# Kernel optimization log

Measured on AMD Instinct MI355X. Metric: run time of the kernel, lower is better.

Reference implementation:

```python
import jax, jax.numpy as jnp
import numpy as np

N = 100000; E = 1600000; G = 512; L = 1000
FXD = 4; FXT = 5; H = 64; NOUT = 2

def setup_inputs() -> dict:
    key = jax.random.key(0)
    ks = jax.random.split(key, 16)
    x = jax.random.normal(ks[0], (N, FXD), dtype=jnp.float32)
    edge_index = jax.random.randint(ks[1], (2, E), 0, N, dtype=jnp.int64)
    # contiguous, non-empty graph assignment (sorted)
    batch = jnp.minimum(jnp.arange(N, dtype=jnp.int64) // (N // G), G - 1)
    target = jax.random.normal(ks[2], (G, L, FXT), dtype=jnp.float32)
    def lin(k, fi, fo):
        s = 1.0 / np.sqrt(fi)
        k1, k2 = jax.random.split(k)
        return (jax.random.uniform(k1, (fi, fo), jnp.float32, -s, s),
                jax.random.uniform(k2, (fo,), jnp.float32, -s, s))
    W1, b1 = lin(ks[3], FXD, H)
    W2, b2 = lin(ks[4], H, 2 * H)
    Wg, bg = lin(ks[5], 2 * H, H)
    s = 1.0 / np.sqrt(FXT * 3)
    Wc = jax.random.uniform(ks[6], (H, FXT, 3), jnp.float32, -s, s)  # OIH
    bc = jax.random.uniform(ks[7], (H,), jnp.float32, -s, s)
    Wt, bt = lin(ks[8], H, H)
    Wf, bf = lin(ks[9], 2 * H, H)
    Wo, bo = lin(ks[10], H, NOUT)
    return dict(x=x, edge_index=edge_index, batch=batch, target=target,
                W1=W1, b1=b1, W2=W2, b2=b2, Wg=Wg, bg=bg,
                Wc=Wc, bc=bc, Wt=Wt, bt=bt, Wf=Wf, bf=bf, Wo=Wo, bo=bo)

def _gcn_prep(edge_index):
    # add self-loops, compute symmetric normalization (PyG gcn_norm)
    loops = jnp.arange(N, dtype=edge_index.dtype)
    row = jnp.concatenate([edge_index[0], loops])
    col = jnp.concatenate([edge_index[1], loops])
    deg = jax.ops.segment_sum(jnp.ones_like(col, dtype=jnp.float32), col, num_segments=N)
    dis = jnp.where(deg > 0, jax.lax.rsqrt(deg), 0.0)
    norm = dis[row] * dis[col]  # [E+N]
    return row, col, norm

def _gcn_conv(h, row, col, norm):
    # gather-scale-scatter aggregation
    msg = h[row] * norm[:, None]
    return jax.ops.segment_sum(msg, col, num_segments=N)

def reference(x, edge_index, batch, target, W1, b1, W2, b2, Wg, bg, Wc, bc, Wt, bt, Wf, bf, Wo, bo):
    row, col, norm = _gcn_prep(edge_index)
    h = jax.nn.relu(_gcn_conv(x @ W1, row, col, norm) + b1)
    h = jax.nn.relu(_gcn_conv(h @ W2, row, col, norm) + b2)
    g = jax.ops.segment_max(h, batch, num_segments=G)  # global_max_pool [G, 2H]
    g = g @ Wg + bg  # dropout = identity (eval)
    t = jnp.transpose(target, (0, 2, 1))  # [G, FXT, L]
    t = jax.lax.conv_general_dilated(t, Wc, (1,), 'VALID',
                                     dimension_numbers=('NCH', 'OIH', 'NCH')) + bc[None, :, None]
    t = jax.nn.relu(t)
    t = jnp.max(t, axis=-1)  # AdaptiveMaxPool1d(1) [G, H]
    t = t @ Wt + bt
    xc = jnp.concatenate([g, t], axis=1)
    xc = jax.nn.relu(xc @ Wf + bf)
    return xc @ Wo + bo
```

## Files before the change

### kernel.cpp

```cpp
#include <hip/hip_runtime.h>
#include <hip/hip_bf16.h>

constexpr int N   = 100000;
constexpr int E   = 1600000;
constexpr int G   = 512;
constexpr int L   = 1000;
constexpr int NPG = 195;

constexpr int SLOTS = 48;
constexpr int NR2   = 256;
constexpr int RS2   = 391;
constexpr int PCAP2 = 6912;
constexpr int BCH   = 4096;
constexpr int NBP   = (E + BCH - 1) / BCH;

typedef __attribute__((ext_vector_type(8))) short bf16x8;
typedef __attribute__((ext_vector_type(4))) float f32x4;

__device__ __forceinline__ float bf2f(__hip_bfloat16 b) { return __bfloat162float(b); }
__device__ __forceinline__ float lo_bf(unsigned v) { return __uint_as_float(v << 16); }
__device__ __forceinline__ float hi_bf(unsigned v) { return __uint_as_float(v & 0xFFFF0000u); }
__device__ __forceinline__ unsigned packbf2(float a, float b) {
    __hip_bfloat16 ha = __float2bfloat16(a), hb = __float2bfloat16(b);
    unsigned short ua = *(unsigned short*)&ha, ub = *(unsigned short*)&hb;
    return (unsigned)ua | ((unsigned)ub << 16);
}

struct SMPart { unsigned rec[BCH]; unsigned char rr[BCH];
                int cnt[NR2]; int base[NR2]; int cur[NR2]; };
struct SMConv { float tg[L * 5]; float pm[4 * 64]; };


__global__ void __launch_bounds__(256) k_part_conv(
        const int* __restrict__ row, const int* __restrict__ col,
        int* __restrict__ pcnt, unsigned* __restrict__ precs,
        const float* __restrict__ target, const float* __restrict__ Wc,
        const float* __restrict__ bc, float* __restrict__ tb,
        const float* __restrict__ W2, short* __restrict__ W2hi,
        short* __restrict__ W2lo) {
    __shared__ __align__(16) char smbuf[sizeof(SMPart) > sizeof(SMConv)
                                        ? sizeof(SMPart) : sizeof(SMConv)];
    int tid = threadIdx.x;
    int bid = blockIdx.x;
    if (bid < NBP) {
        SMPart& sp = *reinterpret_cast<SMPart*>(smbuf);
        sp.cnt[tid] = 0;
        __syncthreads();
        int e0 = bid * BCH;
        int nE = min(BCH, E - e0);
        for (int i = tid; i < nE; i += 256) {
            int c = __builtin_nontemporal_load(col + e0 + i);
            int r = __builtin_nontemporal_load(row + e0 + i);
            int rr = c / RS2;
            sp.rec[i] = ((unsigned)r << 9) | (unsigned)(c - rr * RS2);
            sp.rr[i] = (unsigned char)rr;
            atomicAdd(&sp.cnt[rr], 1);
        }
        __syncthreads();
        sp.base[tid] = atomicAdd(&pcnt[tid], sp.cnt[tid]);
        sp.cur[tid] = 0;
        __syncthreads();
        for (int i = tid; i < nE; i += 256) {
            int rr = sp.rr[i];
            int p = sp.base[rr] + atomicAdd(&sp.cur[rr], 1);
            if (p < PCAP2) precs[rr * PCAP2 + p] = sp.rec[i];
        }
    } else if (bid < NBP + G) {
        SMConv& sc = *reinterpret_cast<SMConv*>(smbuf);
        int gi = bid - NBP;
        const float* tsrc = target + (size_t)gi * (L * 5);
        for (int i = tid; i < L * 5; i += 256) sc.tg[i] = tsrc[i];
        __syncthreads();
        int co = tid & 63, rr = tid >> 6;
        float wc[15];
        #pragma unroll
        for (int j = 0; j < 15; j++) wc[j] = Wc[co * 15 + j];
        const float* tg = sc.tg;
        int p0 = rr * 250;
        int pend = min(p0 + 250, 998);
        float a0 = tg[p0 * 5 + 0], a1 = tg[p0 * 5 + 1], a2 = tg[p0 * 5 + 2],
              a3 = tg[p0 * 5 + 3], a4 = tg[p0 * 5 + 4];
        float b0 = tg[p0 * 5 + 5], b1 = tg[p0 * 5 + 6], b2 = tg[p0 * 5 + 7],
              b3 = tg[p0 * 5 + 8], b4 = tg[p0 * 5 + 9];
        float m = -1e30f;
        for (int p = p0; p < pend; p++) {
            const float* cp = &tg[(p + 2) * 5];
            float c0 = cp[0], c1 = cp[1], c2 = cp[2], c3 = cp[3], c4 = cp[4];
            float v = 0.0f;
            v = fmaf(a0, wc[0],  v); v = fmaf(b0, wc[1],  v); v = fmaf(c0, wc[2],  v);
            v = fmaf(a1, wc[3],  v); v = fmaf(b1, wc[4],  v); v = fmaf(c1, wc[5],  v);
            v = fmaf(a2, wc[6],  v); v = fmaf(b2, wc[7],  v); v = fmaf(c2, wc[8],  v);
            v = fmaf(a3, wc[9],  v); v = fmaf(b3, wc[10], v); v = fmaf(c3, wc[11], v);
            v = fmaf(a4, wc[12], v); v = fmaf(b4, wc[13], v); v = fmaf(c4, wc[14], v);
            m = fmaxf(m, v);
            a0 = b0; a1 = b1; a2 = b2; a3 = b3; a4 = b4;
            b0 = c0; b1 = c1; b2 = c2; b3 = c3; b4 = c4;
        }
        sc.pm[rr * 64 + co] = m;
        __syncthreads();
        if (tid < 64) {
            float mm = fmaxf(fmaxf(sc.pm[tid], sc.pm[64 + tid]),
                             fmaxf(sc.pm[128 + tid], sc.pm[192 + tid]));
            tb[gi * 64 + tid] = fmaxf(mm + bc[tid], 0.0f);
        }
    } else {
        int i = (bid - NBP - G) * 256 + tid;
        if (i < 64 * 128) {
            float w = W2[i];
            __hip_bfloat16 h = __float2bfloat16(w);
            float r = w - __bfloat162float(h);
            __hip_bfloat16 l = __float2bfloat16(r);
            W2hi[i] = *(short*)&h;
            W2lo[i] = *(short*)&l;
        }
    }
}


__global__ void __launch_bounds__(256) k_sort(
        const int* __restrict__ pcnt, const unsigned* __restrict__ precs,
        int* __restrict__ slots, int* __restrict__ cursor, float* __restrict__ dis) {
    __shared__ int cnt2[RS2];
    int tid = threadIdx.x;
    int rr = blockIdx.x;
    int cnt = min(pcnt[rr], PCAP2);
    for (int i = tid; i < RS2; i += 256) cnt2[i] = 0;
    __syncthreads();
    const unsigned* pr = precs + rr * PCAP2;
    for (int i = tid; i < cnt; i += 256) {
        unsigned r = pr[i];
        int ln = (int)(r & 511u);
        int j = atomicAdd(&cnt2[ln], 1);
        if (j < SLOTS) slots[(rr * RS2 + ln) * SLOTS + j] = (int)(r >> 9);
    }
    __syncthreads();
    for (int ln = tid; ln < RS2; ln += 256) {
        int n = rr * RS2 + ln;
        if (n < N) {
            int c = cnt2[ln];
            dis[n] = rsqrtf((float)c + 1.0f);
            cursor[n] = n * SLOTS + min(c, SLOTS);
        }
    }
}


__global__ void __launch_bounds__(256) k_gxl1(
        const int* __restrict__ cursor, const int* __restrict__ slots,
        const float* __restrict__ dis, const float4* __restrict__ x,
        const float* __restrict__ W1, const float* __restrict__ b1,
        unsigned* __restrict__ h32) {
    __shared__ float ax[64][4];
    __shared__ float w1s[256];
    __shared__ float b1s[64];
    int tid = threadIdx.x;
    w1s[tid] = W1[tid];
    if (tid < 64) b1s[tid] = b1[tid];
    int nb = blockIdx.x * 64;
    int ln = tid >> 2, sub = tid & 3;
    int n = nb + ln;
    float4 a = make_float4(0.f, 0.f, 0.f, 0.f);
    if (n < N) {
        int s = n * SLOTS;
        int cnt = cursor[n] - s;
        for (int j = sub; j < cnt; j += 4) {
            int sx = slots[s + j];
            float w = dis[sx];
            float4 v = x[sx];
            a.x = fmaf(v.x, w, a.x); a.y = fmaf(v.y, w, a.y);
            a.z = fmaf(v.z, w, a.z); a.w = fmaf(v.w, w, a.w);
        }
    }
    a.x += __shfl_xor(a.x, 1); a.y += __shfl_xor(a.y, 1);
    a.z += __shfl_xor(a.z, 1); a.w += __shfl_xor(a.w, 1);
    a.x += __shfl_xor(a.x, 2); a.y += __shfl_xor(a.y, 2);
    a.z += __shfl_xor(a.z, 2); a.w += __shfl_xor(a.w, 2);
    if (sub == 0 && n < N) {
        float dn = dis[n];
        float sl = dn * dn;
        float4 xs = x[n];
        ax[ln][0] = fmaf(xs.x, sl, a.x * dn);
        ax[ln][1] = fmaf(xs.y, sl, a.y * dn);
        ax[ln][2] = fmaf(xs.z, sl, a.z * dn);
        ax[ln][3] = fmaf(xs.w, sl, a.w * dn);
    }
    __syncthreads();
    int p = tid & 31, r0 = tid >> 5;
    int f0 = 2 * p, f1 = 2 * p + 1;
    float wA0 = w1s[f0],       wB0 = w1s[f1];
    float wA1 = w1s[64 + f0],  wB1 = w1s[64 + f1];
    float wA2 = w1s[128 + f0], wB2 = w1s[128 + f1];
    float wA3 = w1s[192 + f0], wB3 = w1s[192 + f1];
    float bb0 = b1s[f0], bb1 = b1s[f1];
    #pragma unroll
    for (int i = 0; i < 8; i++) {
        int l2 = r0 + 8 * i;
        int node = nb + l2;
        if (node >= N) break;
        float v0 = bb0, v1 = bb1;
        float g0 = ax[l2][0], g1 = ax[l2][1], g2 = ax[l2][2], g3 = ax[l2][3];
        v0 = fmaf(g0, wA0, v0); v1 = fmaf(g0, wB0, v1);
        v0 = fmaf(g1, wA1, v0); v1 = fmaf(g1, wB1, v1);
        v0 = fmaf(g2, wA2, v0); v1 = fmaf(g2, wB2, v1);
        v0 = fmaf(g3, wA3, v0); v1 = fmaf(g3, wB3, v1);
        h32[(size_t)node * 32 + p] = packbf2(fmaxf(v0, 0.0f), fmaxf(v1, 0.0f));
    }
}


__global__ void __launch_bounds__(256) k_gather_h(
        const int* __restrict__ cursor, const int* __restrict__ slots,
        const float* __restrict__ dis, const unsigned* __restrict__ h32,
        unsigned* __restrict__ aggh32) {
    __shared__ int2 lsw[8][SLOTS];
    __shared__ int  lcnt[8];
    int tid = threadIdx.x;
    int nb = blockIdx.x * 8;
    if (tid < 8) {
        int node = nb + tid;
        lcnt[tid] = (node < N) ? (cursor[node] - node * SLOTS) : 0;
    }
    __syncthreads();
    for (int i = tid; i < 8 * SLOTS; i += 256) {
        int lo = i / SLOTS, j = i - lo * SLOTS;
        if (j < lcnt[lo]) {
            int src = slots[(nb + lo) * SLOTS + j];
            lsw[lo][j] = make_int2(src, __float_as_int(dis[src]));
        }
    }
    __syncthreads();
    int wid = tid >> 6, lane = tid & 63;
    int half = lane >> 5, li = lane & 31;
    int local = wid * 2 + half;
    int n = nb + local;
    if (n >= N) return;
    int cnt = lcnt[local];
    float dn = dis[n];
    float acc0 = 0.0f, acc1 = 0.0f;
    int j = 0;
    for (; j + 16 <= cnt; j += 16) {
        unsigned v[16]; float w[16];
        #pragma unroll
        for (int k = 0; k < 16; k++) {
            int2 e = lsw[local][j + k];
            v[k] = h32[(size_t)e.x * 32 + li];
            w[k] = __int_as_float(e.y);
        }
        #pragma unroll
        for (int k = 0; k < 16; k++) {
            acc0 = fmaf(w[k], lo_bf(v[k]), acc0);
            acc1 = fmaf(w[k], hi_bf(v[k]), acc1);
        }
    }
    for (; j + 4 <= cnt; j += 4) {
        unsigned v[4]; float w[4];
        #pragma unroll
        for (int k = 0; k < 4; k++) {
            int2 e = lsw[local][j + k];
            v[k] = h32[(size_t)e.x * 32 + li];
            w[k] = __int_as_float(e.y);
        }
        #pragma unroll
        for (int k = 0; k < 4; k++) {
            acc0 = fmaf(w[k], lo_bf(v[k]), acc0);
            acc1 = fmaf(w[k], hi_bf(v[k]), acc1);
        }
    }
    for (; j < cnt; j++) {
        int2 e = lsw[local][j];
        unsigned v = h32[(size_t)e.x * 32 + li];
        float w = __int_as_float(e.y);
        acc0 = fmaf(w, lo_bf(v), acc0);
        acc1 = fmaf(w, hi_bf(v), acc1);
    }
    unsigned sv = h32[(size_t)n * 32 + li];
    acc0 = fmaf(dn, lo_bf(sv), acc0) * dn;
    acc1 = fmaf(dn, hi_bf(sv), acc1) * dn;
    aggh32[(size_t)n * 32 + li] = packbf2(acc0, acc1);
}


__global__ void __launch_bounds__(256) k_mfma_pool(
        const __hip_bfloat16* __restrict__ aggh,
        const short* __restrict__ W2hi, const short* __restrict__ W2lo,
        const float* __restrict__ b2, const float* __restrict__ tb,
        const float* __restrict__ Wg, const float* __restrict__ bg,
        const float* __restrict__ Wt, const float* __restrict__ bt,
        const float* __restrict__ Wf, const float* __restrict__ bf,
        const float* __restrict__ Wo, const float* __restrict__ bo,
        float* __restrict__ out) {
    __shared__ float gvec[128], ts[64], g2s[64], t2s[64], xcs[64];
    int tid = threadIdx.x;
    int wid = tid >> 6, lane = tid & 63;
    int m = lane & 15, quad = lane >> 4;
    int gi = blockIdx.x;
    int n0 = gi * NPG;
    int n1 = (gi == G - 1) ? N : n0 + NPG;
    int cb0 = wid * 32, cb1 = cb0 + 16;
    bf16x8 bh[2][2], bl[2][2];
    #pragma unroll
    for (int t = 0; t < 2; t++) {
        int cb = cb0 + t * 16;
        #pragma unroll
        for (int ks = 0; ks < 2; ks++) {
            bf16x8 hh, ll;
            #pragma unroll
            for (int j = 0; j < 8; j++) {
                int k = ks * 32 + quad * 8 + j;
                hh[j] = W2hi[k * 128 + cb + m];
                ll[j] = W2lo[k * 128 + cb + m];
            }
            bh[t][ks] = hh; bl[t][ks] = ll;
        }
    }
    float bias0 = b2[cb0 + m], bias1 = b2[cb1 + m];
    const short* ah = (const short*)aggh;
    float mx0 = 0.0f, mx1 = 0.0f;
    bf16x8 a0, a1;
    {
        const short* p = ah + (size_t)(n0 + m) * 64 + quad * 8;
        a0 = *(const bf16x8*)p;
        a1 = *(const bf16x8*)(p + 32);
    }
    for (int bn = n0; bn < n1; bn += 16) {
        bf16x8 na0 = a0, na1 = a1;
        if (bn + 16 < n1) {
            const short* p = ah + (size_t)(bn + 16 + m) * 64 + quad * 8;
            na0 = *(const bf16x8*)p;
            na1 = *(const bf16x8*)(p + 32);
        }
        f32x4 acc0 = {0.f, 0.f, 0.f, 0.f};
        f32x4 acc1 = {0.f, 0.f, 0.f, 0.f};
        acc0 = __builtin_amdgcn_mfma_f32_16x16x32_bf16(a0, bh[0][0], acc0, 0, 0, 0);
        acc0 = __builtin_amdgcn_mfma_f32_16x16x32_bf16(a1, bh[0][1], acc0, 0, 0, 0);
        acc0 = __builtin_amdgcn_mfma_f32_16x16x32_bf16(a0, bl[0][0], acc0, 0, 0, 0);
        acc0 = __builtin_amdgcn_mfma_f32_16x16x32_bf16(a1, bl[0][1], acc0, 0, 0, 0);
        acc1 = __builtin_amdgcn_mfma_f32_16x16x32_bf16(a0, bh[1][0], acc1, 0, 0, 0);
        acc1 = __builtin_amdgcn_mfma_f32_16x16x32_bf16(a1, bh[1][1], acc1, 0, 0, 0);
        acc1 = __builtin_amdgcn_mfma_f32_16x16x32_bf16(a0, bl[1][0], acc1, 0, 0, 0);
        acc1 = __builtin_amdgcn_mfma_f32_16x16x32_bf16(a1, bl[1][1], acc1, 0, 0, 0);
        int rb = bn + quad * 4;
        #pragma unroll
        for (int r = 0; r < 4; r++) {
            float v0 = fmaxf(acc0[r] + bias0, 0.0f);
            float v1 = fmaxf(acc1[r] + bias1, 0.0f);
            if (rb + r < n1) {
                mx0 = fmaxf(mx0, v0);
                mx1 = fmaxf(mx1, v1);
            }
        }
        a0 = na0; a1 = na1;
    }
    mx0 = fmaxf(mx0, __shfl_xor(mx0, 16));
    mx0 = fmaxf(mx0, __shfl_xor(mx0, 32));
    mx1 = fmaxf(mx1, __shfl_xor(mx1, 16));
    mx1 = fmaxf(mx1, __shfl_xor(mx1, 32));
    if (quad == 0) {
        gvec[cb0 + m] = mx0;
        gvec[cb1 + m] = mx1;
    }
    __syncthreads();
    if (wid == 0) {
        ts[lane] = tb[gi * 64 + lane];
        float a = bg[lane];
        #pragma unroll 8
        for (int k = 0; k < 128; k++) a = fmaf(gvec[k], Wg[k * 64 + lane], a);
        float b = bt[lane];
        #pragma unroll 8
        for (int k = 0; k < 64; k++) b = fmaf(ts[k], Wt[k * 64 + lane], b);
        g2s[lane] = a;
        t2s[lane] = b;
        float c = bf[lane];
        #pragma unroll 8
        for (int k = 0; k < 64; k++) c = fmaf(g2s[k], Wf[k * 64 + lane], c);
        #pragma unroll 8
        for (int k = 0; k < 64; k++) c = fmaf(t2s[k], Wf[(64 + k) * 64 + lane], c);
        xcs[lane] = fmaxf(c, 0.0f);
        if (lane < 2) {
            float o = bo[lane];
            for (int k = 0; k < 64; k++) o = fmaf(xcs[k], Wo[k * 2 + lane], o);
            out[gi * 2 + lane] = o;
        }
    }
}


extern "C" void kernel_launch(void* const* d_in, const int* in_sizes, int n_in,
                              void* d_out, int out_size, void* d_ws, size_t ws_size,
                              hipStream_t stream) {
    const float* x      = (const float*)d_in[0];
    const int*   ei     = (const int*)d_in[1];
    const float* target = (const float*)d_in[3];
    const float* W1 = (const float*)d_in[4];
    const float* b1 = (const float*)d_in[5];
    const float* W2 = (const float*)d_in[6];
    const float* b2 = (const float*)d_in[7];
    const float* Wg = (const float*)d_in[8];
    const float* bg = (const float*)d_in[9];
    const float* Wc = (const float*)d_in[10];
    const float* bc = (const float*)d_in[11];
    const float* Wt = (const float*)d_in[12];
    const float* bt = (const float*)d_in[13];
    const float* Wf = (const float*)d_in[14];
    const float* bf = (const float*)d_in[15];
    const float* Wo = (const float*)d_in[16];
    const float* bo = (const float*)d_in[17];
    float* out = (float*)d_out;

    const int* row = ei;
    const int* col = ei + E;

    char* base = (char*)d_ws;
    size_t o = 0;
    auto alloc = [&](size_t bytes) -> void* {
        void* p = base + o;
        o = (o + bytes + 255) & ~(size_t)255;
        return p;
    };
    int*      cursor = (int*)     alloc((size_t)N * 4);
    float*    dis    = (float*)   alloc((size_t)N * 4);
    int*      slots  = (int*)     alloc((size_t)N * SLOTS * 4);
    int*      pcnt   = (int*)     alloc(NR2 * 4);
    unsigned* precs  = (unsigned*)alloc((size_t)NR2 * PCAP2 * 4);
    __hip_bfloat16* h    = (__hip_bfloat16*)alloc((size_t)N * 64 * 2);
    __hip_bfloat16* aggh = (__hip_bfloat16*)alloc((size_t)N * 64 * 2);
    short*    W2hi   = (short*)   alloc((size_t)64 * 128 * 2);
    short*    W2lo   = (short*)   alloc((size_t)64 * 128 * 2);
    float*    tb     = (float*)   alloc((size_t)G * 64 * 4);
    (void)    alloc(4096);

    (void)hipMemsetAsync(pcnt, 0, NR2 * 4, stream);
    k_part_conv<<<NBP + G + 32, 256, 0, stream>>>(row, col, pcnt, precs,
                                                  target, Wc, bc, tb,
                                                  W2, W2hi, W2lo);
    k_sort     <<<NR2, 256, 0, stream>>>(pcnt, precs, slots, cursor, dis);
    k_gxl1     <<<(N + 63) / 64, 256, 0, stream>>>(cursor, slots, dis,
                                                   (const float4*)x, W1, b1,
                                                   (unsigned*)h);
    k_gather_h <<<(N + 7) / 8, 256, 0, stream>>>(cursor, slots, dis,
                                                 (const unsigned*)h, (unsigned*)aggh);
    k_mfma_pool<<<G, 256, 0, stream>>>(aggh, W2hi, W2lo, b2, tb, Wg, bg, Wt, bt,
                                       Wf, bf, Wo, bo, out);
}
```

Before: 234.8 us.

## Slice hidden features into four planes for cache-local gather aggregation

Layer-1 output h is now stored in four feature-slice planes of 16 bf16 values (32 bytes) each, instead of one 128-byte row per node. The gather kernel launches four blocks per 32-node group, each reading only one slice, so the gathered working set per pass is a quarter of the full array and fits caches better. The cost is reloading the slot lists and dis values four times and issuing narrower 32-byte random reads per edge.

```diff
diff --git a/kernel.cpp b/kernel.cpp
--- a/kernel.cpp
+++ b/kernel.cpp
@@ -13,6 +13,8 @@
 constexpr int PCAP2 = 6912;
 constexpr int BCH   = 4096;
 constexpr int NBP   = (E + BCH - 1) / BCH;
+
+constexpr int NSL = 4;
 
 typedef __attribute__((ext_vector_type(8))) short bf16x8;
 typedef __attribute__((ext_vector_type(4))) float f32x4;
@@ -192,6 +194,7 @@
     float wA2 = w1s[128 + f0], wB2 = w1s[128 + f1];
     float wA3 = w1s[192 + f0], wB3 = w1s[192 + f1];
     float bb0 = b1s[f0], bb1 = b1s[f1];
+    size_t sbase = (size_t)(p >> 3) * N * 8 + (p & 7);
     #pragma unroll
     for (int i = 0; i < 8; i++) {
         int l2 = r0 + 8 * i;
@@ -203,39 +206,42 @@
         v0 = fmaf(g1, wA1, v0); v1 = fmaf(g1, wB1, v1);
         v0 = fmaf(g2, wA2, v0); v1 = fmaf(g2, wB2, v1);
         v0 = fmaf(g3, wA3, v0); v1 = fmaf(g3, wB3, v1);
-        h32[(size_t)node * 32 + p] = packbf2(fmaxf(v0, 0.0f), fmaxf(v1, 0.0f));
-    }
-}
-
-
-__global__ void __launch_bounds__(256) k_gather_h(
+        h32[sbase + (size_t)node * 8] = packbf2(fmaxf(v0, 0.0f), fmaxf(v1, 0.0f));
+    }
+}
+
+
+__global__ void __launch_bounds__(256) k_gather_hs(
         const int* __restrict__ cursor, const int* __restrict__ slots,
-        const float* __restrict__ dis, const unsigned* __restrict__ h32,
+        const float* __restrict__ dis, const unsigned* __restrict__ h32s,
         unsigned* __restrict__ aggh32) {
-    __shared__ int2 lsw[8][SLOTS];
-    __shared__ int  lcnt[8];
+    __shared__ int2 lsw[32][SLOTS];
+    __shared__ int  lcnt[32];
     int tid = threadIdx.x;
-    int nb = blockIdx.x * 8;
-    if (tid < 8) {
+    int slice = blockIdx.x & (NSL - 1);
+    int nb = (blockIdx.x >> 2) * 32;
+    if (tid < 32) {
         int node = nb + tid;
         lcnt[tid] = (node < N) ? (cursor[node] - node * SLOTS) : 0;
     }
     __syncthreads();
-    for (int i = tid; i < 8 * SLOTS; i += 256) {
+    for (int i = tid; i < 32 * SLOTS; i += 256) {
         int lo = i / SLOTS, j = i - lo * SLOTS;
         if (j < lcnt[lo]) {
-            int src = slots[(nb + lo) * SLOTS + j];
+            int src = slots[(size_t)(nb + lo) * SLOTS + j];
             lsw[lo][j] = make_int2(src, __float_as_int(dis[src]));
         }
     }
     __syncthreads();
     int wid = tid >> 6, lane = tid & 63;
-    int half = lane >> 5, li = lane & 31;
-    int local = wid * 2 + half;
+    int local = wid * 8 + (lane >> 3);
+    int d = lane & 3 | (lane & 7);
+    d = lane & 7;
     int n = nb + local;
     if (n >= N) return;
     int cnt = lcnt[local];
     float dn = dis[n];
+    const unsigned* hp = h32s + (size_t)slice * N * 8;
     float acc0 = 0.0f, acc1 = 0.0f;
     int j = 0;
     for (; j + 16 <= cnt; j += 16) {
@@ -243,7 +249,7 @@
         #pragma unroll
         for (int k = 0; k < 16; k++) {
             int2 e = lsw[local][j + k];
-            v[k] = h32[(size_t)e.x * 32 + li];
+            v[k] = hp[(size_t)e.x * 8 + d];
             w[k] = __int_as_float(e.y);
         }
         #pragma unroll
@@ -257,7 +263,7 @@
         #pragma unroll
         for (int k = 0; k < 4; k++) {
             int2 e = lsw[local][j + k];
-            v[k] = h32[(size_t)e.x * 32 + li];
+            v[k] = hp[(size_t)e.x * 8 + d];
             w[k] = __int_as_float(e.y);
         }
         #pragma unroll
@@ -268,15 +274,15 @@
     }
     for (; j < cnt; j++) {
         int2 e = lsw[local][j];
-        unsigned v = h32[(size_t)e.x * 32 + li];
+        unsigned v = hp[(size_t)e.x * 8 + d];
         float w = __int_as_float(e.y);
         acc0 = fmaf(w, lo_bf(v), acc0);
         acc1 = fmaf(w, hi_bf(v), acc1);
     }
-    unsigned sv = h32[(size_t)n * 32 + li];
+    unsigned sv = hp[(size_t)n * 8 + d];
     acc0 = fmaf(dn, lo_bf(sv), acc0) * dn;
     acc1 = fmaf(dn, hi_bf(sv), acc1) * dn;
-    aggh32[(size_t)n * 32 + li] = packbf2(acc0, acc1);
+    aggh32[(size_t)n * 32 + slice * 8 + d] = packbf2(acc0, acc1);
 }
 
 
@@ -437,7 +443,7 @@
     k_gxl1     <<<(N + 63) / 64, 256, 0, stream>>>(cursor, slots, dis,
                                                    (const float4*)x, W1, b1,
                                                    (unsigned*)h);
-    k_gather_h <<<(N + 7) / 8, 256, 0, stream>>>(cursor, slots, dis,
+    k_gather_hs<<<((N + 31) / 32) * NSL, 256, 0, stream>>>(cursor, slots, dis,
                                                  (const unsigned*)h, (unsigned*)aggh);
     k_mfma_pool<<<G, 256, 0, stream>>>(aggh, W2hi, W2lo, b2, tb, Wg, bg, Wt, bt,
                                        Wf, bf, Wo, bo, out);
```

Measured after the change: 266.3 us. +13.4%, slower.

## Replace two-pass bucket partition and sort with direct global-atomic slot scatter

Applied to the files above, without the earlier changes.

Drops the shared-memory bucket partition and the separate per-bucket sort kernel. Each edge now does a global atomicAdd on its destination's counter and writes its source straight into a fixed-slot CSR. The dis array is gone; normalization is recomputed from the counts with rsqrtf in the consumer kernels. This saves one kernel launch and the staging buffer traffic, but adds contended global atomics and scattered writes, plus an extra dependent count load per neighbor.

```diff
diff --git a/kernel.cpp b/kernel.cpp
--- a/kernel.cpp
+++ b/kernel.cpp
@@ -8,16 +8,11 @@
 constexpr int NPG = 195;
 
 constexpr int SLOTS = 48;
-constexpr int NR2   = 256;
-constexpr int RS2   = 391;
-constexpr int PCAP2 = 6912;
-constexpr int BCH   = 4096;
-constexpr int NBP   = (E + BCH - 1) / BCH;
+constexpr int SCT   = 1536;
 
 typedef __attribute__((ext_vector_type(8))) short bf16x8;
 typedef __attribute__((ext_vector_type(4))) float f32x4;
 
-__device__ __forceinline__ float bf2f(__hip_bfloat16 b) { return __bfloat162float(b); }
 __device__ __forceinline__ float lo_bf(unsigned v) { return __uint_as_float(v << 16); }
 __device__ __forceinline__ float hi_bf(unsigned v) { return __uint_as_float(v & 0xFFFF0000u); }
 __device__ __forceinline__ unsigned packbf2(float a, float b) {
@@ -26,56 +21,34 @@
     return (unsigned)ua | ((unsigned)ub << 16);
 }
 
-struct SMPart { unsigned rec[BCH]; unsigned char rr[BCH];
-                int cnt[NR2]; int base[NR2]; int cur[NR2]; };
-struct SMConv { float tg[L * 5]; float pm[4 * 64]; };
-
-
-__global__ void __launch_bounds__(256) k_part_conv(
+
+__global__ void __launch_bounds__(256) k_scatter_conv(
         const int* __restrict__ row, const int* __restrict__ col,
-        int* __restrict__ pcnt, unsigned* __restrict__ precs,
+        int* __restrict__ cnt, int* __restrict__ slots,
         const float* __restrict__ target, const float* __restrict__ Wc,
         const float* __restrict__ bc, float* __restrict__ tb,
         const float* __restrict__ W2, short* __restrict__ W2hi,
         short* __restrict__ W2lo) {
-    __shared__ __align__(16) char smbuf[sizeof(SMPart) > sizeof(SMConv)
-                                        ? sizeof(SMPart) : sizeof(SMConv)];
+    __shared__ float tg[L * 5];
+    __shared__ float pm[4 * 64];
     int tid = threadIdx.x;
     int bid = blockIdx.x;
-    if (bid < NBP) {
-        SMPart& sp = *reinterpret_cast<SMPart*>(smbuf);
-        sp.cnt[tid] = 0;
-        __syncthreads();
-        int e0 = bid * BCH;
-        int nE = min(BCH, E - e0);
-        for (int i = tid; i < nE; i += 256) {
-            int c = __builtin_nontemporal_load(col + e0 + i);
-            int r = __builtin_nontemporal_load(row + e0 + i);
-            int rr = c / RS2;
-            sp.rec[i] = ((unsigned)r << 9) | (unsigned)(c - rr * RS2);
-            sp.rr[i] = (unsigned char)rr;
-            atomicAdd(&sp.cnt[rr], 1);
-        }
-        __syncthreads();
-        sp.base[tid] = atomicAdd(&pcnt[tid], sp.cnt[tid]);
-        sp.cur[tid] = 0;
-        __syncthreads();
-        for (int i = tid; i < nE; i += 256) {
-            int rr = sp.rr[i];
-            int p = sp.base[rr] + atomicAdd(&sp.cur[rr], 1);
-            if (p < PCAP2) precs[rr * PCAP2 + p] = sp.rec[i];
-        }
-    } else if (bid < NBP + G) {
-        SMConv& sc = *reinterpret_cast<SMConv*>(smbuf);
-        int gi = bid - NBP;
+    if (bid < SCT) {
+        for (int e = bid * 256 + tid; e < E; e += SCT * 256) {
+            int c = __builtin_nontemporal_load(col + e);
+            int r = __builtin_nontemporal_load(row + e);
+            int j = atomicAdd(&cnt[c], 1);
+            if (j < SLOTS) slots[c * SLOTS + j] = r;
+        }
+    } else if (bid < SCT + G) {
+        int gi = bid - SCT;
         const float* tsrc = target + (size_t)gi * (L * 5);
-        for (int i = tid; i < L * 5; i += 256) sc.tg[i] = tsrc[i];
+        for (int i = tid; i < L * 5; i += 256) tg[i] = tsrc[i];
         __syncthreads();
         int co = tid & 63, rr = tid >> 6;
         float wc[15];
         #pragma unroll
         for (int j = 0; j < 15; j++) wc[j] = Wc[co * 15 + j];
-        const float* tg = sc.tg;
         int p0 = rr * 250;
         int pend = min(p0 + 250, 998);
         float a0 = tg[p0 * 5 + 0], a1 = tg[p0 * 5 + 1], a2 = tg[p0 * 5 + 2],
@@ -96,15 +69,15 @@
             a0 = b0; a1 = b1; a2 = b2; a3 = b3; a4 = b4;
             b0 = c0; b1 = c1; b2 = c2; b3 = c3; b4 = c4;
         }
-        sc.pm[rr * 64 + co] = m;
+        pm[rr * 64 + co] = m;
         __syncthreads();
         if (tid < 64) {
-            float mm = fmaxf(fmaxf(sc.pm[tid], sc.pm[64 + tid]),
-                             fmaxf(sc.pm[128 + tid], sc.pm[192 + tid]));
+            float mm = fmaxf(fmaxf(pm[tid], pm[64 + tid]),
+                             fmaxf(pm[128 + tid], pm[192 + tid]));
             tb[gi * 64 + tid] = fmaxf(mm + bc[tid], 0.0f);
         }
     } else {
-        int i = (bid - NBP - G) * 256 + tid;
+        int i = (bid - SCT - G) * 256 + tid;
         if (i < 64 * 128) {
             float w = W2[i];
             __hip_bfloat16 h = __float2bfloat16(w);
@@ -117,37 +90,9 @@
 }
 
 
-__global__ void __launch_bounds__(256) k_sort(
-        const int* __restrict__ pcnt, const unsigned* __restrict__ precs,
-        int* __restrict__ slots, int* __restrict__ cursor, float* __restrict__ dis) {
-    __shared__ int cnt2[RS2];
-    int tid = threadIdx.x;
-    int rr = blockIdx.x;
-    int cnt = min(pcnt[rr], PCAP2);
-    for (int i = tid; i < RS2; i += 256) cnt2[i] = 0;
-    __syncthreads();
-    const unsigned* pr = precs + rr * PCAP2;
-    for (int i = tid; i < cnt; i += 256) {
-        unsigned r = pr[i];
-        int ln = (int)(r & 511u);
-        int j = atomicAdd(&cnt2[ln], 1);
-        if (j < SLOTS) slots[(rr * RS2 + ln) * SLOTS + j] = (int)(r >> 9);
-    }
-    __syncthreads();
-    for (int ln = tid; ln < RS2; ln += 256) {
-        int n = rr * RS2 + ln;
-        if (n < N) {
-            int c = cnt2[ln];
-            dis[n] = rsqrtf((float)c + 1.0f);
-            cursor[n] = n * SLOTS + min(c, SLOTS);
-        }
-    }
-}
-
-
 __global__ void __launch_bounds__(256) k_gxl1(
-        const int* __restrict__ cursor, const int* __restrict__ slots,
-        const float* __restrict__ dis, const float4* __restrict__ x,
+        const int* __restrict__ cnt, const int* __restrict__ slots,
+        const float4* __restrict__ x,
         const float* __restrict__ W1, const float* __restrict__ b1,
         unsigned* __restrict__ h32) {
     __shared__ float ax[64][4];
@@ -160,12 +105,14 @@
     int ln = tid >> 2, sub = tid & 3;
     int n = nb + ln;
     float4 a = make_float4(0.f, 0.f, 0.f, 0.f);
+    int rawc = 0;
     if (n < N) {
+        rawc = cnt[n];
+        int c = min(rawc, SLOTS);
         int s = n * SLOTS;
-        int cnt = cursor[n] - s;
-        for (int j = sub; j < cnt; j += 4) {
+        for (int j = sub; j < c; j += 4) {
             int sx = slots[s + j];
-            float w = dis[sx];
+            float w = rsqrtf((float)cnt[sx] + 1.0f);
             float4 v = x[sx];
             a.x = fmaf(v.x, w, a.x); a.y = fmaf(v.y, w, a.y);
             a.z = fmaf(v.z, w, a.z); a.w = fmaf(v.w, w, a.w);
@@ -176,7 +123,7 @@
     a.x += __shfl_xor(a.x, 2); a.y += __shfl_xor(a.y, 2);
     a.z += __shfl_xor(a.z, 2); a.w += __shfl_xor(a.w, 2);
     if (sub == 0 && n < N) {
-        float dn = dis[n];
+        float dn = rsqrtf((float)rawc + 1.0f);
         float sl = dn * dn;
         float4 xs = x[n];
         ax[ln][0] = fmaf(xs.x, sl, a.x * dn);
@@ -209,23 +156,26 @@
 
 
 __global__ void __launch_bounds__(256) k_gather_h(
-        const int* __restrict__ cursor, const int* __restrict__ slots,
-        const float* __restrict__ dis, const unsigned* __restrict__ h32,
-        unsigned* __restrict__ aggh32) {
+        const int* __restrict__ cnt, const int* __restrict__ slots,
+        const unsigned* __restrict__ h32, unsigned* __restrict__ aggh32) {
     __shared__ int2 lsw[8][SLOTS];
     __shared__ int  lcnt[8];
+    __shared__ float ldn[8];
     int tid = threadIdx.x;
     int nb = blockIdx.x * 8;
     if (tid < 8) {
         int node = nb + tid;
-        lcnt[tid] = (node < N) ? (cursor[node] - node * SLOTS) : 0;
+        int rawc = (node < N) ? cnt[node] : 0;
+        lcnt[tid] = min(rawc, SLOTS);
+        ldn[tid] = rsqrtf((float)rawc + 1.0f);
     }
     __syncthreads();
     for (int i = tid; i < 8 * SLOTS; i += 256) {
         int lo = i / SLOTS, j = i - lo * SLOTS;
         if (j < lcnt[lo]) {
             int src = slots[(nb + lo) * SLOTS + j];
-            lsw[lo][j] = make_int2(src, __float_as_int(dis[src]));
+            lsw[lo][j] = make_int2(src,
+                __float_as_int(rsqrtf((float)cnt[src] + 1.0f)));
         }
     }
     __syncthreads();
@@ -234,11 +184,11 @@
     int local = wid * 2 + half;
     int n = nb + local;
     if (n >= N) return;
-    int cnt = lcnt[local];
-    float dn = dis[n];
+    int c = lcnt[local];
+    float dn = ldn[local];
     float acc0 = 0.0f, acc1 = 0.0f;
     int j = 0;
-    for (; j + 16 <= cnt; j += 16) {
+    for (; j + 16 <= c; j += 16) {
         unsigned v[16]; float w[16];
         #pragma unroll
         for (int k = 0; k < 16; k++) {
@@ -252,7 +202,7 @@
             acc1 = fmaf(w[k], hi_bf(v[k]), acc1);
         }
     }
-    for (; j + 4 <= cnt; j += 4) {
+    for (; j + 4 <= c; j += 4) {
         unsigned v[4]; float w[4];
         #pragma unroll
         for (int k = 0; k < 4; k++) {
@@ -266,7 +216,7 @@
             acc1 = fmaf(w[k], hi_bf(v[k]), acc1);
         }
     }
-    for (; j < cnt; j++) {
+    for (; j < c; j++) {
         int2 e = lsw[local][j];
         unsigned v = h32[(size_t)e.x * 32 + li];
         float w = __int_as_float(e.y);
@@ -417,11 +367,8 @@
         o = (o + bytes + 255) & ~(size_t)255;
         return p;
     };
-    int*      cursor = (int*)     alloc((size_t)N * 4);
-    float*    dis    = (float*)   alloc((size_t)N * 4);
+    int*      cnt    = (int*)     alloc((size_t)N * 4);
     int*      slots  = (int*)     alloc((size_t)N * SLOTS * 4);
-    int*      pcnt   = (int*)     alloc(NR2 * 4);
-    unsigned* precs  = (unsigned*)alloc((size_t)NR2 * PCAP2 * 4);
     __hip_bfloat16* h    = (__hip_bfloat16*)alloc((size_t)N * 64 * 2);
     __hip_bfloat16* aggh = (__hip_bfloat16*)alloc((size_t)N * 64 * 2);
     short*    W2hi   = (short*)   alloc((size_t)64 * 128 * 2);
@@ -429,15 +376,14 @@
     float*    tb     = (float*)   alloc((size_t)G * 64 * 4);
     (void)    alloc(4096);
 
-    (void)hipMemsetAsync(pcnt, 0, NR2 * 4, stream);
-    k_part_conv<<<NBP + G + 32, 256, 0, stream>>>(row, col, pcnt, precs,
-                                                  target, Wc, bc, tb,
-                                                  W2, W2hi, W2lo);
-    k_sort     <<<NR2, 256, 0, stream>>>(pcnt, precs, slots, cursor, dis);
-    k_gxl1     <<<(N + 63) / 64, 256, 0, stream>>>(cursor, slots, dis,
+    (void)hipMemsetAsync(cnt, 0, (size_t)N * 4, stream);
+    k_scatter_conv<<<SCT + G + 32, 256, 0, stream>>>(row, col, cnt, slots,
+                                                     target, Wc, bc, tb,
+                                                     W2, W2hi, W2lo);
+    k_gxl1     <<<(N + 63) / 64, 256, 0, stream>>>(cnt, slots,
                                                    (const float4*)x, W1, b1,
                                                    (unsigned*)h);
-    k_gather_h <<<(N + 7) / 8, 256, 0, stream>>>(cursor, slots, dis,
+    k_gather_h <<<(N + 7) / 8, 256, 0, stream>>>(cnt, slots,
                                                  (const unsigned*)h, (unsigned*)aggh);
     k_mfma_pool<<<G, 256, 0, stream>>>(aggh, W2hi, W2lo, b2, tb, Wg, bg, Wt, bt,
                                        Wf, bf, Wo, bo, out);
```

Result: slower. 316.1 us (+34.6%).
